# Optimization experiments

Measured on AMD Instinct MI355X. Metric: run time of the kernel, lower is better.

The kernel has to match this reference:

```python
import jax, jax.numpy as jnp
import numpy as np

DIM = 768
HEADS = 12
HEAD_DIM = DIM // HEADS
B, N = 4, 2048


def setup_inputs() -> dict:
    key = jax.random.key(0)
    ks = jax.random.split(key, 5)
    s = 0.02
    return {
        "x": jax.random.normal(ks[0], (B, N, DIM), dtype=jnp.float32),
        "w_qkv": jax.random.normal(ks[1], (DIM, 3 * DIM), dtype=jnp.float32) * s,
        "b_qkv": jnp.zeros((3 * DIM,), dtype=jnp.float32),
        "w_proj": jax.random.normal(ks[2], (DIM, DIM), dtype=jnp.float32) * s,
        "b_proj": jnp.zeros((DIM,), dtype=jnp.float32),
    }


def reference(x, w_qkv, b_qkv, w_proj, b_proj):
    b, n, c = x.shape
    scale = HEAD_DIM ** -0.5
    qkv = x @ w_qkv + b_qkv                       # [B,N,3C]
    qkv = qkv.reshape(b, n, 3, HEADS, HEAD_DIM)
    q = qkv[:, :, 0].transpose(0, 2, 1, 3)        # [B,H,N,D]
    k = qkv[:, :, 1].transpose(0, 2, 1, 3)
    v = qkv[:, :, 2].transpose(0, 2, 1, 3)
    attn = jnp.einsum("bhqd,bhkd->bhqk", q, k) * scale
    attn = jax.nn.softmax(attn, axis=-1)
    out = jnp.einsum("bhqk,bhkd->bhqd", attn, v)  # [B,H,N,D]
    out = out.transpose(0, 2, 1, 3).reshape(b, n, c)
    return out @ w_proj + b_proj
```

## Files before the change

### kernel.cpp

```cpp
#include <hip/hip_runtime.h>

typedef short sh8 __attribute__((ext_vector_type(8)));
typedef short sh4 __attribute__((ext_vector_type(4)));
typedef float f32x4 __attribute__((ext_vector_type(4)));
typedef float f32x16 __attribute__((ext_vector_type(16)));
typedef unsigned u32x4 __attribute__((ext_vector_type(4)));

extern "C" __device__ float __ocml_native_exp2_f32(float);

__device__ __forceinline__ short f2bf(float f) {
  unsigned u = __builtin_bit_cast(unsigned, f);
  u += 0x7fffu + ((u >> 16) & 1u);
  return (short)(u >> 16);
}

__device__ __forceinline__ void gload16(const short* g, short* l) {
  __builtin_amdgcn_global_load_lds(
      (const __attribute__((address_space(1))) unsigned*)g,
      (__attribute__((address_space(3))) unsigned*)l, 16, 0, 0);
}

__device__ __forceinline__ void wait2_barrier() {
  asm volatile("s_waitcnt vmcnt(2)" ::: "memory");
  __builtin_amdgcn_s_barrier();
  asm volatile("" ::: "memory");
}
__device__ __forceinline__ void wait0_barrier() {
  asm volatile("s_waitcnt vmcnt(0)" ::: "memory");
  __builtin_amdgcn_s_barrier();
  asm volatile("" ::: "memory");
}

__device__ __forceinline__ int xcd_swizzle(int bidl, int nwg) {
  int q = nwg >> 3, rr = nwg & 7;
  int xcd = bidl & 7, idx = bidl >> 3;
  return (xcd < rr ? xcd * (q + 1) : rr * (q + 1) + (xcd - rr) * q) + idx;
}

__global__ void cast_f32_bf16(const float* __restrict__ in, short* __restrict__ out, int n) {
  int i = (blockIdx.x * blockDim.x + threadIdx.x) * 4;
  if (i >= n) return;
  float4 f = *(const float4*)(in + i);
  sh4 o;
  o.x = f2bf(f.x); o.y = f2bf(f.y); o.z = f2bf(f.z); o.w = f2bf(f.w);
  *(sh4*)(out + i) = o;
}

__global__ __launch_bounds__(256) void transpose_cast_t(
    const float* __restrict__ in, short* __restrict__ out, int K, int Nn) {
  __shared__ short Tl[64][72];
  const int t = threadIdx.x;
  const int n0 = blockIdx.x * 64, k0 = blockIdx.y * 64;
  const int kr0 = t >> 4;
  const int nc = (t & 15) * 4;
#pragma unroll
  for (int p = 0; p < 4; p++) {
    int kr = kr0 + p * 16;
    float4 f = *(const float4*)(in + (size_t)(k0 + kr) * Nn + n0 + nc);
    Tl[nc + 0][kr] = f2bf(f.x);
    Tl[nc + 1][kr] = f2bf(f.y);
    Tl[nc + 2][kr] = f2bf(f.z);
    Tl[nc + 3][kr] = f2bf(f.w);
  }
  __syncthreads();
  const int nr0 = t >> 3;
  const int kk = (t & 7) * 8;
#pragma unroll
  for (int p = 0; p < 2; p++) {
    int nr = nr0 + p * 32;
    *(sh8*)(out + (size_t)(n0 + nr) * K + k0 + kk) = *(const sh8*)&Tl[nr][kk];
  }
}

template <int OUTF32>
__global__ __launch_bounds__(256, 4) void gemm_bt(
    const short* __restrict__ A, const short* __restrict__ Bt,
    const float* __restrict__ bias, void* __restrict__ Cv,
    int M, int Nn, int K) {
  __shared__ short SMEM[20480];
  const int t = threadIdx.x;
  const int wave = t >> 6, lane = t & 63, quad = lane >> 4, l15 = lane & 15;
  const int wm = (wave >> 1) * 64, wn = (wave & 1) * 64;
  const int nwg = gridDim.x * gridDim.y;
  const int wg = xcd_swizzle(blockIdx.y * gridDim.x + blockIdx.x, nwg);
  const int row0 = (wg / gridDim.x) * 128, col0 = (wg % gridDim.x) * 128;
  f32x4 acc[4][4] = {};

  const int srow = t >> 2;
  const int ssl = ((t & 3) ^ ((t >> 3) & 3)) * 8;
  const short* Asrc0 = A + (size_t)(row0 + srow) * K + ssl;
  const short* Asrc1 = A + (size_t)(row0 + 64 + srow) * K + ssl;
  const short* Bsrc0 = Bt + (size_t)(col0 + srow) * K + ssl;
  const short* Bsrc1 = Bt + (size_t)(col0 + 64 + srow) * K + ssl;
  short* AsF = SMEM;
  short* BsF = SMEM + 12288;
  const int wdst = wave * 512;

  const int soA = (quad ^ ((l15 >> 1) & 3)) * 8;

  const int T = K >> 5;
  gload16(Asrc0, AsF + wdst);
  gload16(Asrc1, AsF + 2048 + wdst);
  gload16(Bsrc0, BsF + wdst);
  gload16(Bsrc1, BsF + 2048 + wdst);
  gload16(Asrc0 + 32, AsF + 4096 + wdst);
  gload16(Asrc1 + 32, AsF + 4096 + 2048 + wdst);

  int ra = 0, wa = 2;
  for (int tt = 0; tt < T; tt++) {
    if (tt + 1 < T) wait2_barrier(); else wait0_barrier();
    if (tt + 1 < T) {
      const int k0 = (tt + 1) * 32;
      short* Bd = BsF + ((tt + 1) & 1) * 4096 + wdst;
      gload16(Bsrc0 + k0, Bd);
      gload16(Bsrc1 + k0, Bd + 2048);
    }
    if (tt + 2 < T) {
      const int k0 = (tt + 2) * 32;
      short* Ad = AsF + wa * 4096 + wdst;
      gload16(Asrc0 + k0, Ad);
      gload16(Asrc1 + k0, Ad + 2048);
    }
    const short* Ab = AsF + ra * 4096;
    const short* Bb = BsF + (tt & 1) * 4096;
    sh8 af[4], bfv[4];
#pragma unroll
    for (int i = 0; i < 4; i++) af[i] = *(const sh8*)&Ab[(wm + i * 16 + l15) * 32 + soA];
#pragma unroll
    for (int j = 0; j < 4; j++) bfv[j] = *(const sh8*)&Bb[(wn + j * 16 + l15) * 32 + soA];
#pragma unroll
    for (int i = 0; i < 4; i++)
#pragma unroll
      for (int j = 0; j < 4; j++)
        acc[i][j] = __builtin_amdgcn_mfma_f32_16x16x32_bf16(af[i], bfv[j], acc[i][j], 0, 0, 0);
    ra = ra == 2 ? 0 : ra + 1;
    wa = wa == 2 ? 0 : wa + 1;
  }

#pragma unroll
  for (int i = 0; i < 4; i++)
#pragma unroll
    for (int j = 0; j < 4; j++) {
      int r = row0 + wm + i * 16 + quad * 4;
      int c = col0 + wn + j * 16 + l15;
      float bv = bias[c];
#pragma unroll
      for (int e = 0; e < 4; e++) {
        float v = acc[i][j][e] + bv;
        if (OUTF32)
          ((float*)Cv)[(size_t)(r + e) * Nn + c] = v;
        else
          ((short*)Cv)[(size_t)(r + e) * Nn + c] = f2bf(v);
      }
    }
}

__global__ __launch_bounds__(256, 4) void gemm_qkv(
    const short* __restrict__ A, const short* __restrict__ Bt,
    const float* __restrict__ bias,
    short* __restrict__ Qh, short* __restrict__ Kh, short* __restrict__ VhT) {
  const int K = 768;
  __shared__ short SMEM[20480];
  const int t = threadIdx.x;
  const int wave = t >> 6, lane = t & 63, quad = lane >> 4, l15 = lane & 15;
  const int wm = (wave >> 1) * 64, wn = (wave & 1) * 64;
  const int nwg = gridDim.x * gridDim.y;
  const int wg = xcd_swizzle(blockIdx.y * gridDim.x + blockIdx.x, nwg);
  const int row0 = (wg / gridDim.x) * 128, col0 = (wg % gridDim.x) * 128;
  f32x4 acc[4][4] = {};

  const int srow = t >> 2;
  const int ssl = ((t & 3) ^ ((t >> 3) & 3)) * 8;
  const short* Asrc0 = A + (size_t)(row0 + srow) * K + ssl;
  const short* Asrc1 = A + (size_t)(row0 + 64 + srow) * K + ssl;
  const short* Bsrc0 = Bt + (size_t)(col0 + srow) * K + ssl;
  const short* Bsrc1 = Bt + (size_t)(col0 + 64 + srow) * K + ssl;
  short* AsF = SMEM;
  short* BsF = SMEM + 12288;
  const int wdst = wave * 512;

  const int soA = (quad ^ ((l15 >> 1) & 3)) * 8;

  const int T = K >> 5;
  gload16(Asrc0, AsF + wdst);
  gload16(Asrc1, AsF + 2048 + wdst);
  gload16(Bsrc0, BsF + wdst);
  gload16(Bsrc1, BsF + 2048 + wdst);
  gload16(Asrc0 + 32, AsF + 4096 + wdst);
  gload16(Asrc1 + 32, AsF + 4096 + 2048 + wdst);

  int ra = 0, wa = 2;
  for (int tt = 0; tt < T; tt++) {
    if (tt + 1 < T) wait2_barrier(); else wait0_barrier();
    if (tt + 1 < T) {
      const int k0 = (tt + 1) * 32;
      short* Bd = BsF + ((tt + 1) & 1) * 4096 + wdst;
      gload16(Bsrc0 + k0, Bd);
      gload16(Bsrc1 + k0, Bd + 2048);
    }
    if (tt + 2 < T) {
      const int k0 = (tt + 2) * 32;
      short* Ad = AsF + wa * 4096 + wdst;
      gload16(Asrc0 + k0, Ad);
      gload16(Asrc1 + k0, Ad + 2048);
    }
    const short* Ab = AsF + ra * 4096;
    const short* Bb = BsF + (tt & 1) * 4096;
    sh8 af[4], bfv[4];
#pragma unroll
    for (int i = 0; i < 4; i++) af[i] = *(const sh8*)&Ab[(wm + i * 16 + l15) * 32 + soA];
#pragma unroll
    for (int j = 0; j < 4; j++) bfv[j] = *(const sh8*)&Bb[(wn + j * 16 + l15) * 32 + soA];
#pragma unroll
    for (int i = 0; i < 4; i++)
#pragma unroll
      for (int j = 0; j < 4; j++)
        acc[i][j] = __builtin_amdgcn_mfma_f32_16x16x32_bf16(af[i], bfv[j], acc[i][j], 0, 0, 0);
    ra = ra == 2 ? 0 : ra + 1;
    wa = wa == 2 ? 0 : wa + 1;
  }

  const int s = col0 >= 1536 ? 2 : (col0 >= 768 ? 1 : 0);

  if (s < 2) {
    short* dst = s == 0 ? Qh : Kh;
    const float scl = (s == 0) ? 0.18033688011112042f : 1.0f;
#pragma unroll
    for (int j = 0; j < 4; j++) {
      int c = col0 + wn + j * 16 + l15;
      int hd = c - s * 768;
      int h = hd >> 6;
      float bv = bias[c];
#pragma unroll
      for (int i = 0; i < 4; i++) {
        int rbase = row0 + wm + i * 16 + quad * 4;
#pragma unroll
        for (int e = 0; e < 4; e++) {
          int r = rbase + e;
          int b = r >> 11, n = r & 2047;
          float v = (acc[i][j][e] + bv) * scl;
          dst[(size_t)(b * 12 + h) * 131072 + n * 64 + (hd & 63)] = f2bf(v);
        }
      }
    }
  } else {
    __syncthreads();
    short* Tl = SMEM;
#pragma unroll
    for (int j = 0; j < 4; j++) {
      int cl = wn + j * 16 + l15;
      float bv = bias[col0 + cl];
#pragma unroll
      for (int i = 0; i < 4; i++) {
        int rl = wm + i * 16 + quad * 4;
        sh4 pk;
#pragma unroll
        for (int e = 0; e < 4; e++) pk[e] = f2bf(acc[i][j][e] + bv);
        *(sh4*)&Tl[cl * 136 + rl] = pk;
      }
    }
    __syncthreads();
    const int b = row0 >> 11, n0 = row0 & 2047;
    const int h0 = (col0 - 1536) >> 6;
#pragma unroll
    for (int p = 0; p < 8; p++) {
      int cl = (t >> 4) + p * 16;
      int nn = (t & 15) * 8;
      int hg = h0 + (cl >> 6);
      int d = cl & 63;
      sh8 vv = *(const sh8*)&Tl[cl * 136 + nn];
      *(sh8*)&VhT[(size_t)(b * 12 + hg) * 131072 + (size_t)d * 2048 + n0 + nn] = vv;
    }
  }
}

__global__ __launch_bounds__(256, 4) void attn8(const short* __restrict__ Qh,
                                                const short* __restrict__ Kh,
                                                const short* __restrict__ VhT,
                                                short* __restrict__ outb) {
  const int bid = blockIdx.x;
  const int qb = bid / 48;
  const int bh = bid - qb * 48;
  const int t = threadIdx.x;
  const int w = t >> 6, lane = t & 63;
  const int l31 = lane & 31, hi = lane >> 5;

  __shared__ short SM[20480];

  const size_t hb = (size_t)bh * 131072;

  sh8 qa[4];
  {
    const short* qp = Qh + hb + (size_t)(qb * 128 + w * 32 + l31) * 64 + hi * 8;
    qa[0] = *(const sh8*)(qp);
    qa[1] = *(const sh8*)(qp + 16);
    qa[2] = *(const sh8*)(qp + 32);
    qa[3] = *(const sh8*)(qp + 48);
  }
  asm volatile("s_waitcnt vmcnt(0)" ::: "memory");

  f32x16 o[2] = {};
  f32x4 lsv = {};

  const int srow = t >> 3;
  const int ssl = ((t & 7) ^ (srow & 7)) * 8;
  const short* Ksrc = Kh + hb + (size_t)srow * 64 + ssl;
  const short* Vsrc = VhT + hb + (size_t)srow * 2048 + ssl;
  short* KlF = SM;
  short* VtF = SM + 12288;
  const int wdst = w * 512;

  const int sw7 = l31 & 7;
  int rsl[4];
#pragma unroll
  for (int ks = 0; ks < 4; ks++) rsl[ks] = (((ks << 1) | hi) ^ sw7) * 8;

  gload16(Ksrc, KlF + wdst);
  gload16(Ksrc + (size_t)32 * 64, KlF + 2048 + wdst);
  gload16(Vsrc, VtF + wdst);
  gload16(Vsrc + (size_t)32 * 2048, VtF + 2048 + wdst);
  gload16(Ksrc + (size_t)64 * 64, KlF + 4096 + wdst);
  gload16(Ksrc + (size_t)96 * 64, KlF + 4096 + 2048 + wdst);

  int rk = 0, wk = 2;
  for (int kt = 0; kt < 32; kt++) {
    if (kt < 31) wait2_barrier(); else wait0_barrier();
    if (kt + 1 < 32) {
      const int key0 = (kt + 1) * 64;
      short* Vd = VtF + ((kt + 1) & 1) * 4096 + wdst;
      gload16(Vsrc + key0, Vd);
      gload16(Vsrc + (size_t)32 * 2048 + key0, Vd + 2048);
    }
    if (kt + 2 < 32) {
      const int key0 = (kt + 2) * 64;
      short* Kd = KlF + wk * 4096 + wdst;
      gload16(Ksrc + (size_t)key0 * 64, Kd);
      gload16(Ksrc + (size_t)(key0 + 32) * 64, Kd + 2048);
    }

    const short* Kb = KlF + rk * 4096;
    const short* Vb = VtF + (kt & 1) * 4096;

    sh8 pa[4];
#pragma unroll
    for (int kb = 0; kb < 2; kb++) {
      const short* kr = Kb + (kb * 32 + l31) * 64;
      f32x16 s = {};
#pragma unroll
      for (int ks = 0; ks < 4; ks++)
        s = __builtin_amdgcn_mfma_f32_32x32x16_bf16(*(const sh8*)(kr + rsl[ks]), qa[ks], s, 0, 0, 0);
      unsigned u[8];
#pragma unroll
      for (int m = 0; m < 8; m++) {
        float e0 = __ocml_native_exp2_f32(s[2 * m]);
        float e1 = __ocml_native_exp2_f32(s[2 * m + 1]);
        lsv[m & 3] += e0 + e1;
        asm("v_cvt_pk_bf16_f32 %0, %1, %2" : "=v"(u[m]) : "v"(e0), "v"(e1));
      }
      unsigned y0 = (unsigned)__shfl_xor((int)(hi ? u[0] : u[2]), 32, 64);
      unsigned y1 = (unsigned)__shfl_xor((int)(hi ? u[1] : u[3]), 32, 64);
      unsigned y2 = (unsigned)__shfl_xor((int)(hi ? u[4] : u[6]), 32, 64);
      unsigned y3 = (unsigned)__shfl_xor((int)(hi ? u[5] : u[7]), 32, 64);
      unsigned w0 = hi ? y0 : u[0];
      unsigned w1 = hi ? y1 : u[1];
      unsigned w2 = hi ? u[2] : y0;
      unsigned w3 = hi ? u[3] : y1;
      unsigned w4 = hi ? y2 : u[4];
      unsigned w5 = hi ? y3 : u[5];
      unsigned w6 = hi ? u[6] : y2;
      unsigned w7 = hi ? u[7] : y3;
      u32x4 A0 = {w0, w1, w2, w3};
      u32x4 A1 = {w4, w5, w6, w7};
      pa[2 * kb] = __builtin_bit_cast(sh8, A0);
      pa[2 * kb + 1] = __builtin_bit_cast(sh8, A1);
    }

    __builtin_amdgcn_s_setprio(1);
#pragma unroll
    for (int db = 0; db < 2; db++) {
      const short* vr = Vb + (db * 32 + l31) * 64;
#pragma unroll
      for (int ks = 0; ks < 4; ks++)
        o[db] = __builtin_amdgcn_mfma_f32_32x32x16_bf16(pa[ks], *(const sh8*)(vr + rsl[ks]), o[db], 0, 0, 0);
    }
    __builtin_amdgcn_s_setprio(0);
    rk = rk == 2 ? 0 : rk + 1;
    wk = wk == 2 ? 0 : wk + 1;
  }

  float ls = lsv[0] + lsv[1] + lsv[2] + lsv[3];
  ls += __shfl_xor(ls, 32, 64);
  float inv = 1.f / ls;

  const int b = bh / 12, hh = bh - b * 12;
#pragma unroll
  for (int r = 0; r < 16; r++) {
    int qr = (r & 3) + 8 * (r >> 2) + 4 * hi;
    float iv = __shfl(inv, qr, 64);
    int n = qb * 128 + w * 32 + qr;
    short* op = outb + (size_t)(b * 2048 + n) * 768 + hh * 64 + l31;
    op[0] = f2bf(o[0][r] * iv);
    op[32] = f2bf(o[1][r] * iv);
  }
}

extern "C" void kernel_launch(void* const* d_in, const int* in_sizes, int n_in,
                              void* d_out, int out_size, void* d_ws, size_t ws_size,
                              hipStream_t stream) {
  const float* x = (const float*)d_in[0];
  const float* w_qkv = (const float*)d_in[1];
  const float* b_qkv = (const float*)d_in[2];
  const float* w_proj = (const float*)d_in[3];
  const float* b_proj = (const float*)d_in[4];
  float* out = (float*)d_out;

  char* p = (char*)d_ws;
  short* xb = (short*)p;     p += (size_t)8192 * 768 * 2;
  short* wqkvT = (short*)p;  p += (size_t)2304 * 768 * 2;
  short* wprojT = (short*)p; p += (size_t)768 * 768 * 2;
  short* Qh = (short*)p;     p += (size_t)48 * 131072 * 2;
  short* Kh = (short*)p;     p += (size_t)48 * 131072 * 2;
  short* VhT = (short*)p;    p += (size_t)48 * 131072 * 2;
  short* attnb = (short*)p;  p += (size_t)8192 * 768 * 2;

  cast_f32_bf16<<<(8192 * 768 / 4) / 256, 256, 0, stream>>>(x, xb, 8192 * 768);
  {
    dim3 gt(2304 / 64, 768 / 64);
    transpose_cast_t<<<gt, 256, 0, stream>>>(w_qkv, wqkvT, 768, 2304);
  }
  {
    dim3 gt(768 / 64, 768 / 64);
    transpose_cast_t<<<gt, 256, 0, stream>>>(w_proj, wprojT, 768, 768);
  }

  dim3 g1(2304 / 128, 8192 / 128);
  gemm_qkv<<<g1, 256, 0, stream>>>(xb, wqkvT, b_qkv, Qh, Kh, VhT);

  attn8<<<16 * 48, 256, 0, stream>>>(Qh, Kh, VhT, attnb);

  dim3 g2(768 / 128, 8192 / 128);
  gemm_bt<1><<<g2, 256, 0, stream>>>(attnb, wprojT, b_proj, out, 8192, 768, 768);
}
```

Baseline: 215.9 us.

## Split attention keys across two wave groups and shrink projection GEMM tile

The attention kernel now launches 512 threads per block. Two groups of four waves each process half of the key sequence with their own LDS buffers, then merge partial outputs and row sums through shared memory before normalising and storing. The output projection GEMM uses 64x128 tiles instead of 128x128, doubling the block count and using a single A stream with a 1-deep wait. Both changes aim to raise occupancy and parallelism on a small grid. The cost is extra LDS traffic, a block-wide merge step, and less data reuse per GEMM block. The attention merge only holds if the per-group softmax uses the same max reference.

Measured after the change: 222.6 us. +3.1%, slower.

```diff
diff --git a/kernel.cpp b/kernel.cpp
--- a/kernel.cpp
+++ b/kernel.cpp
@@ -22,6 +22,11 @@
 
 __device__ __forceinline__ void wait2_barrier() {
   asm volatile("s_waitcnt vmcnt(2)" ::: "memory");
+  __builtin_amdgcn_s_barrier();
+  asm volatile("" ::: "memory");
+}
+__device__ __forceinline__ void wait1_barrier() {
+  asm volatile("s_waitcnt vmcnt(1)" ::: "memory");
   __builtin_amdgcn_s_barrier();
   asm volatile("" ::: "memory");
 }
@@ -77,38 +82,35 @@
     const short* __restrict__ A, const short* __restrict__ Bt,
     const float* __restrict__ bias, void* __restrict__ Cv,
     int M, int Nn, int K) {
-  __shared__ short SMEM[20480];
+  __shared__ short SMEM[14336];
   const int t = threadIdx.x;
   const int wave = t >> 6, lane = t & 63, quad = lane >> 4, l15 = lane & 15;
-  const int wm = (wave >> 1) * 64, wn = (wave & 1) * 64;
+  const int wm = (wave >> 1) * 32, wn = (wave & 1) * 64;
   const int nwg = gridDim.x * gridDim.y;
   const int wg = xcd_swizzle(blockIdx.y * gridDim.x + blockIdx.x, nwg);
-  const int row0 = (wg / gridDim.x) * 128, col0 = (wg % gridDim.x) * 128;
-  f32x4 acc[4][4] = {};
+  const int row0 = (wg / gridDim.x) * 64, col0 = (wg % gridDim.x) * 128;
+  f32x4 acc[2][4] = {};
 
   const int srow = t >> 2;
   const int ssl = ((t & 3) ^ ((t >> 3) & 3)) * 8;
   const short* Asrc0 = A + (size_t)(row0 + srow) * K + ssl;
-  const short* Asrc1 = A + (size_t)(row0 + 64 + srow) * K + ssl;
   const short* Bsrc0 = Bt + (size_t)(col0 + srow) * K + ssl;
   const short* Bsrc1 = Bt + (size_t)(col0 + 64 + srow) * K + ssl;
   short* AsF = SMEM;
-  short* BsF = SMEM + 12288;
+  short* BsF = SMEM + 6144;
   const int wdst = wave * 512;
 
   const int soA = (quad ^ ((l15 >> 1) & 3)) * 8;
 
   const int T = K >> 5;
   gload16(Asrc0, AsF + wdst);
-  gload16(Asrc1, AsF + 2048 + wdst);
   gload16(Bsrc0, BsF + wdst);
   gload16(Bsrc1, BsF + 2048 + wdst);
-  gload16(Asrc0 + 32, AsF + 4096 + wdst);
-  gload16(Asrc1 + 32, AsF + 4096 + 2048 + wdst);
+  gload16(Asrc0 + 32, AsF + 2048 + wdst);
 
   int ra = 0, wa = 2;
   for (int tt = 0; tt < T; tt++) {
-    if (tt + 1 < T) wait2_barrier(); else wait0_barrier();
+    if (tt + 1 < T) wait1_barrier(); else wait0_barrier();
     if (tt + 1 < T) {
       const int k0 = (tt + 1) * 32;
       short* Bd = BsF + ((tt + 1) & 1) * 4096 + wdst;
@@ -116,20 +118,17 @@
       gload16(Bsrc1 + k0, Bd + 2048);
     }
     if (tt + 2 < T) {
-      const int k0 = (tt + 2) * 32;
-      short* Ad = AsF + wa * 4096 + wdst;
-      gload16(Asrc0 + k0, Ad);
-      gload16(Asrc1 + k0, Ad + 2048);
-    }
-    const short* Ab = AsF + ra * 4096;
+      gload16(Asrc0 + (tt + 2) * 32, AsF + wa * 2048 + wdst);
+    }
+    const short* Ab = AsF + ra * 2048;
     const short* Bb = BsF + (tt & 1) * 4096;
-    sh8 af[4], bfv[4];
-#pragma unroll
-    for (int i = 0; i < 4; i++) af[i] = *(const sh8*)&Ab[(wm + i * 16 + l15) * 32 + soA];
+    sh8 af[2], bfv[4];
+#pragma unroll
+    for (int i = 0; i < 2; i++) af[i] = *(const sh8*)&Ab[(wm + i * 16 + l15) * 32 + soA];
 #pragma unroll
     for (int j = 0; j < 4; j++) bfv[j] = *(const sh8*)&Bb[(wn + j * 16 + l15) * 32 + soA];
 #pragma unroll
-    for (int i = 0; i < 4; i++)
+    for (int i = 0; i < 2; i++)
 #pragma unroll
       for (int j = 0; j < 4; j++)
         acc[i][j] = __builtin_amdgcn_mfma_f32_16x16x32_bf16(af[i], bfv[j], acc[i][j], 0, 0, 0);
@@ -138,7 +137,7 @@
   }
 
 #pragma unroll
-  for (int i = 0; i < 4; i++)
+  for (int i = 0; i < 2; i++)
 #pragma unroll
     for (int j = 0; j < 4; j++) {
       int r = row0 + wm + i * 16 + quad * 4;
@@ -274,7 +273,7 @@
   }
 }
 
-__global__ __launch_bounds__(256, 4) void attn8(const short* __restrict__ Qh,
+__global__ __launch_bounds__(512, 4) void attn9(const short* __restrict__ Qh,
                                                 const short* __restrict__ Kh,
                                                 const short* __restrict__ VhT,
                                                 short* __restrict__ outb) {
@@ -283,15 +282,16 @@
   const int bh = bid - qb * 48;
   const int t = threadIdx.x;
   const int w = t >> 6, lane = t & 63;
+  const int wl = w & 3, g = w >> 2;
   const int l31 = lane & 31, hi = lane >> 5;
 
-  __shared__ short SM[20480];
+  __shared__ short SM[40960];
 
   const size_t hb = (size_t)bh * 131072;
 
   sh8 qa[4];
   {
-    const short* qp = Qh + hb + (size_t)(qb * 128 + w * 32 + l31) * 64 + hi * 8;
+    const short* qp = Qh + hb + (size_t)(qb * 128 + wl * 32 + l31) * 64 + hi * 8;
     qa[0] = *(const sh8*)(qp);
     qa[1] = *(const sh8*)(qp + 16);
     qa[2] = *(const sh8*)(qp + 32);
@@ -302,13 +302,14 @@
   f32x16 o[2] = {};
   f32x4 lsv = {};
 
-  const int srow = t >> 3;
-  const int ssl = ((t & 7) ^ (srow & 7)) * 8;
-  const short* Ksrc = Kh + hb + (size_t)srow * 64 + ssl;
-  const short* Vsrc = VhT + hb + (size_t)srow * 2048 + ssl;
-  short* KlF = SM;
-  short* VtF = SM + 12288;
-  const int wdst = w * 512;
+  const int tg = t & 255;
+  const int srow = tg >> 3;
+  const int ssl = ((tg & 7) ^ (srow & 7)) * 8;
+  const short* Ksrc = Kh + hb + (size_t)(g * 1024 + srow) * 64 + ssl;
+  const short* Vsrc = VhT + hb + (size_t)srow * 2048 + g * 1024 + ssl;
+  short* KlF = SM + g * 20480;
+  short* VtF = KlF + 12288;
+  const int wdst = wl * 512;
 
   const int sw7 = l31 & 7;
   int rsl[4];
@@ -323,15 +324,15 @@
   gload16(Ksrc + (size_t)96 * 64, KlF + 4096 + 2048 + wdst);
 
   int rk = 0, wk = 2;
-  for (int kt = 0; kt < 32; kt++) {
-    if (kt < 31) wait2_barrier(); else wait0_barrier();
-    if (kt + 1 < 32) {
+  for (int kt = 0; kt < 16; kt++) {
+    if (kt < 15) wait2_barrier(); else wait0_barrier();
+    if (kt + 1 < 16) {
       const int key0 = (kt + 1) * 64;
       short* Vd = VtF + ((kt + 1) & 1) * 4096 + wdst;
       gload16(Vsrc + key0, Vd);
       gload16(Vsrc + (size_t)32 * 2048 + key0, Vd + 2048);
     }
-    if (kt + 2 < 32) {
+    if (kt + 2 < 16) {
       const int key0 = (kt + 2) * 64;
       short* Kd = KlF + wk * 4096 + wdst;
       gload16(Ksrc + (size_t)key0 * 64, Kd);
@@ -390,17 +391,38 @@
 
   float ls = lsv[0] + lsv[1] + lsv[2] + lsv[3];
   ls += __shfl_xor(ls, 32, 64);
-  float inv = 1.f / ls;
-
-  const int b = bh / 12, hh = bh - b * 12;
-#pragma unroll
-  for (int r = 0; r < 16; r++) {
-    int qr = (r & 3) + 8 * (r >> 2) + 4 * hi;
-    float iv = __shfl(inv, qr, 64);
-    int n = qb * 128 + w * 32 + qr;
-    short* op = outb + (size_t)(b * 2048 + n) * 768 + hh * 64 + l31;
-    op[0] = f2bf(o[0][r] * iv);
-    op[32] = f2bf(o[1][r] * iv);
+
+  __syncthreads();
+  float* cb = (float*)SM;
+  const int ci = (wl * 64 + lane) * 33;
+  if (g == 1) {
+#pragma unroll
+    for (int r = 0; r < 16; r++) {
+      cb[ci + r] = o[0][r];
+      cb[ci + 16 + r] = o[1][r];
+    }
+    cb[ci + 32] = ls;
+  }
+  __syncthreads();
+  if (g == 0) {
+#pragma unroll
+    for (int r = 0; r < 16; r++) {
+      o[0][r] += cb[ci + r];
+      o[1][r] += cb[ci + 16 + r];
+    }
+    ls += cb[ci + 32];
+    float inv = 1.f / ls;
+
+    const int b = bh / 12, hh = bh - b * 12;
+#pragma unroll
+    for (int r = 0; r < 16; r++) {
+      int qr = (r & 3) + 8 * (r >> 2) + 4 * hi;
+      float iv = __shfl(inv, qr, 64);
+      int n = qb * 128 + wl * 32 + qr;
+      short* op = outb + (size_t)(b * 2048 + n) * 768 + hh * 64 + l31;
+      op[0] = f2bf(o[0][r] * iv);
+      op[32] = f2bf(o[1][r] * iv);
+    }
   }
 }
 
@@ -436,8 +458,8 @@
   dim3 g1(2304 / 128, 8192 / 128);
   gemm_qkv<<<g1, 256, 0, stream>>>(xb, wqkvT, b_qkv, Qh, Kh, VhT);
 
-  attn8<<<16 * 48, 256, 0, stream>>>(Qh, Kh, VhT, attnb);
-
-  dim3 g2(768 / 128, 8192 / 128);
+  attn9<<<16 * 48, 512, 0, stream>>>(Qh, Kh, VhT, attnb);
+
+  dim3 g2(768 / 128, 8192 / 64);
   gemm_bt<1><<<g2, 256, 0, stream>>>(attnb, wprojT, b_proj, out, 8192, 768, 768);
 }
```
